# Kernel tuning notes

Hardware: AMD Instinct MI355X
Metric: run time of the kernel (lower is better)

Reference implementation:

```python
import jax, jax.numpy as jnp
import numpy as np

N_NODES = 50000
N_EDGES = 800000
FEAT = 64
HID = 128
N_TYPES = 4
N_REL = 3
N_LAYERS = 2
LN_EPS = 1e-5


def setup_inputs() -> dict:
    key = jax.random.key(0)
    ks = jax.random.split(key, 20)
    inp = {
        "z": jax.random.randint(ks[0], (N_NODES,), 0, 100, dtype=jnp.int32),
        "node_type": jax.random.randint(ks[1], (N_NODES,), 0, N_TYPES, dtype=jnp.int32),
        "edge_index": jax.random.randint(ks[2], (2, N_EDGES), 0, N_NODES, dtype=jnp.int32),
        "edge_type": jax.random.randint(ks[3], (N_EDGES,), 0, N_REL, dtype=jnp.int32),
        # learned parameters
        "z_embed": jax.random.normal(ks[4], (100, FEAT), jnp.float32),
        "enc_w1": jax.random.normal(ks[5], (N_TYPES, FEAT, HID), jnp.float32) * 0.05,
        "enc_b1": jnp.zeros((N_TYPES, HID), jnp.float32),
        "enc_w2": jax.random.normal(ks[6], (N_TYPES, HID, HID), jnp.float32) * 0.05,
        "enc_b2": jnp.zeros((N_TYPES, HID), jnp.float32),
        "lin_w": jax.random.normal(ks[7], (N_LAYERS, HID, HID), jnp.float32) * 0.05,
        "lin_b": jnp.zeros((N_LAYERS, HID), jnp.float32),
        "rel_w": jax.random.normal(ks[8], (N_LAYERS, N_REL, HID, HID), jnp.float32) * 0.05,
        "ln_g": jnp.ones((N_LAYERS, HID), jnp.float32),
        "ln_b": jnp.zeros((N_LAYERS, HID), jnp.float32),
        "reg_w": jax.random.normal(ks[9], (HID, 1), jnp.float32) * 0.05,
        "reg_b": jnp.zeros((1,), jnp.float32),
    }
    return inp


def _layer_norm(x, g, b):
    mu = jnp.mean(x, axis=-1, keepdims=True)
    var = jnp.mean((x - mu) ** 2, axis=-1, keepdims=True)
    return (x - mu) * jax.lax.rsqrt(var + LN_EPS) * g + b


def reference(z, node_type, edge_index, edge_type, z_embed, enc_w1, enc_b1,
              enc_w2, enc_b2, lin_w, lin_b, rel_w, ln_g, ln_b, reg_w, reg_b):
    n = z.shape[0]
    # FeatureBuilder (site_ads=None path): atomic-number embedding lookup
    raw = z_embed[z]  # [N, FEAT]
    # TypeSpecificEncoder: run all 4 type MLPs, select per node by node_type
    h = jax.nn.relu(jnp.einsum('nd,tdh->nth', raw, enc_w1) + enc_b1)  # [N,T,H]
    enc_all = jnp.einsum('nth,tho->nto', h, enc_w2) + enc_b2           # [N,T,H]
    x = jnp.take_along_axis(enc_all, node_type[:, None, None].astype(jnp.int32), axis=1)[:, 0, :]

    src, dst = edge_index[0], edge_index[1]
    deg = jax.ops.segment_sum(jnp.ones((edge_type.shape[0],), x.dtype), dst, num_segments=n)
    deg = jnp.clip(deg, 1.0, None)[:, None]  # [N,1]

    for l in range(N_LAYERS):
        out = jnp.zeros_like(x)
        x_src = x[src]  # [E, H] gathered source features
        for r in range(N_REL):
            mask = (edge_type == r).astype(x.dtype)[:, None]
            msg = (x_src * mask) @ rel_w[l, r]  # [E, H]
            out = out + jax.ops.segment_sum(msg, dst, num_segments=n)
        out = out / deg
        x = _layer_norm(x @ lin_w[l] + lin_b[l] + out, ln_g[l], ln_b[l])

    pooled = jnp.mean(x, axis=0)  # mean pooling, mask = all ones
    return pooled @ reg_w + reg_b  # [1]
```

## Files before the change

### kernel.cpp

```cpp
#include <hip/hip_runtime.h>

#define N_NODES 50000
#define N_EDGES 800000
#define FEAT 64
#define HID 128
#define N_TYPES 4
#define N_REL 3
#define N_LAYERS 2
#define LN_EPS 1e-5f
#define NROWS 50016
#define NG32 1563
#define CAP 64
#define NBKT 196
#define CAP1 4608
#define EPB 4096
#define BINCAP 56
#define NCOMBO 400
#define WT_STRIDE 136

typedef __attribute__((ext_vector_type(8))) short bf16x8;
typedef __attribute__((ext_vector_type(16))) float f32x16;
typedef __attribute__((ext_vector_type(2))) float f32x2;

static __device__ inline unsigned short f2bf(float f) {
    unsigned int u = __float_as_uint(f);
    return (unsigned short)((u + 0x7fffu + ((u >> 16) & 1u)) >> 16);
}
static __device__ inline unsigned int packbf2(float lo, float hi) {
    return (unsigned int)f2bf(lo) | ((unsigned int)f2bf(hi) << 16);
}

static __device__ inline void acc8_fp8w(float* a, unsigned int wx, unsigned int wy) {
    f32x2 d0 = __builtin_amdgcn_cvt_pk_f32_fp8((int)wx, false);
    f32x2 d1 = __builtin_amdgcn_cvt_pk_f32_fp8((int)wx, true);
    f32x2 d2 = __builtin_amdgcn_cvt_pk_f32_fp8((int)wy, false);
    f32x2 d3 = __builtin_amdgcn_cvt_pk_f32_fp8((int)wy, true);
    a[0] += d0[0]; a[1] += d0[1]; a[2] += d1[0]; a[3] += d1[1];
    a[4] += d2[0]; a[5] += d2[1]; a[6] += d3[0]; a[7] += d3[1];
}
static __device__ inline void acc16_fp8(float* a, uint4 w) {
    acc8_fp8w(a, w.x, w.y);
    acc8_fp8w(a + 8, w.z, w.w);
}

__global__ __launch_bounds__(256) void build_tables_kernel(
    const int* __restrict__ src, const int* __restrict__ dst,
    const int* __restrict__ et, const int* __restrict__ z,
    const int* __restrict__ nt,
    const float* __restrict__ z_embed, const float* __restrict__ w1,
    const float* __restrict__ b1, const float* __restrict__ w2,
    const float* __restrict__ b2, const float* __restrict__ rel_w,
    const float* __restrict__ lin_w, const float* __restrict__ lin_b,
    unsigned short* __restrict__ combo, int* __restrict__ bcnt,
    int* __restrict__ bucket, unsigned int* __restrict__ ytab,
    float* __restrict__ lintab, unsigned short* __restrict__ wbuf,
    float* __restrict__ pooled) {
    __shared__ int lbin[NBKT * BINCAP];
    __shared__ int lcnt[NBKT];
    __shared__ int lbase[NBKT];
    __shared__ float h[HID];
    __shared__ float xrow[HID];
    __shared__ float tmp[HID];

    int b = blockIdx.x;
    if (b < NBKT) {
        int ci = b * 256 + threadIdx.x;
        if (ci < N_NODES) combo[ci] = (unsigned short)(z[ci] * 4 + nt[ci]);
        for (int i = threadIdx.x; i < NBKT; i += 256) lcnt[i] = 0;
        __syncthreads();
        int base = b * EPB;
#pragma unroll
        for (int i = 0; i < EPB / 256; ++i) {
            int e = base + i * 256 + threadIdx.x;
            if (e < N_EDGES) {
                int d = dst[e];
                int bk = d >> 8;
                int v = src[e] | (et[e] << 16) | ((d & 255) << 18);
                int pos = atomicAdd(&lcnt[bk], 1);
                if (pos < BINCAP) lbin[bk * BINCAP + pos] = v;
            }
        }
        __syncthreads();
        if (threadIdx.x < NBKT) {
            int c = min(lcnt[threadIdx.x], BINCAP);
            lcnt[threadIdx.x] = c;
            lbase[threadIdx.x] = atomicAdd(&bcnt[threadIdx.x], c);
        }
        __syncthreads();
        int wv = threadIdx.x >> 6, ln = threadIdx.x & 63;
        for (int bb = wv; bb < NBKT; bb += 4) {
            int c = lcnt[bb];
            if (ln < c) {
                int gp = lbase[bb] + ln;
                if (gp < CAP1) bucket[bb * CAP1 + gp] = lbin[bb * BINCAP + ln];
            }
        }
        return;
    }
    if (b >= NBKT + NCOMBO) {
        int pb = b - (NBKT + NCOMBO);
        if (pb == 0 && threadIdx.x < HID) pooled[threadIdx.x] = 0.0f;
        int idx = pb * 256 + threadIdx.x;
        int k = idx & 127;
        int col = (idx >> 7) & 127;
        int mat = idx >> 14;
        float w = (mat < 3) ? rel_w[(((size_t)(3 + mat)) * HID + k) * HID + col]
                            : lin_w[((size_t)(HID + k)) * HID + col];
        wbuf[(size_t)mat * HID * WT_STRIDE + col * WT_STRIDE + k] = f2bf(w);
        return;
    }
    int c = b - NBKT;
    int zi = c >> 2;
    int t = c & 3;
    int j = threadIdx.x;
    bool act = j < HID;
    if (act) {
        float acc = b1[t * HID + j];
#pragma unroll 8
        for (int k = 0; k < FEAT; ++k)
            acc = fmaf(z_embed[zi * FEAT + k], w1[((size_t)t * FEAT + k) * HID + j], acc);
        h[j] = fmaxf(acc, 0.0f);
    }
    __syncthreads();
    if (act) {
        float acc2 = b2[t * HID + j];
#pragma unroll 8
        for (int k = 0; k < HID; ++k)
            acc2 = fmaf(h[k], w2[(size_t)t * HID * HID + k * HID + j], acc2);
        xrow[j] = acc2;
    }
    __syncthreads();
#pragma unroll 1
    for (int r = 0; r < N_REL; ++r) {
        if (act) {
            float a = 0.f;
            const float* W = rel_w + (size_t)r * HID * HID;
#pragma unroll 8
            for (int k = 0; k < HID; ++k) a = fmaf(xrow[k], W[k * HID + j], a);
            tmp[j] = a;
        }
        __syncthreads();
        if (j < 32) {
            int w0 = __builtin_amdgcn_cvt_pk_fp8_f32(tmp[4 * j], tmp[4 * j + 1], 0, false);
            w0 = __builtin_amdgcn_cvt_pk_fp8_f32(tmp[4 * j + 2], tmp[4 * j + 3], w0, true);
            ytab[(r * NCOMBO + c) * 32 + j] = (unsigned)w0;
        }
        __syncthreads();
    }
    if (act) {
        float a = lin_b[j];
#pragma unroll 8
        for (int k = 0; k < HID; ++k) a = fmaf(xrow[k], lin_w[k * HID + j], a);
        lintab[c * HID + j] = a;
    }
}

__global__ __launch_bounds__(256) void build2_kernel(const int* __restrict__ bcnt,
                                                     const int* __restrict__ bucket,
                                                     const unsigned short* __restrict__ combo,
                                                     int* __restrict__ cnt3,
                                                     int* __restrict__ payload) {
    __shared__ int lcnt[256 * 3];
    for (int i = threadIdx.x; i < 768; i += 256) lcnt[i] = 0;
    __syncthreads();
    int b = blockIdx.x;
    int n0 = b << 8;
    int cb = min(bcnt[b], CAP1);
    const int* bk = bucket + b * CAP1;
    for (int i = threadIdx.x; i < cb; i += 256) {
        int v = bk[i];
        atomicAdd(&lcnt[((v >> 18) & 255) * 3 + ((v >> 16) & 3)], 1);
    }
    __syncthreads();
    int t = threadIdx.x;
    int c0 = min(lcnt[t * 3 + 0], CAP);
    int c1 = min(lcnt[t * 3 + 1], CAP - c0);
    int c2 = min(lcnt[t * 3 + 2], CAP - c0 - c1);
    __syncthreads();
    lcnt[t * 3 + 0] = 0;
    lcnt[t * 3 + 1] = c0;
    lcnt[t * 3 + 2] = c0 + c1;
    int node = n0 + t;
    if (node < N_NODES) cnt3[node] = c0 | (c1 << 8) | (c2 << 16);
    __syncthreads();
    for (int i = threadIdx.x; i < cb; i += 256) {
        int v = bk[i];
        int dl = (v >> 18) & 255;
        int r = (v >> 16) & 3;
        int sc = v & 0xffff;
        int pos = atomicAdd(&lcnt[dl * 3 + r], 1);
        if (pos < CAP)
            payload[((n0 + dl) << 6) + pos] = sc | ((int)combo[sc] << 18);
    }
}

__global__ __launch_bounds__(256) void gather_ln1_kernel(
    const int* __restrict__ cnt3, const int* __restrict__ payload,
    const uint4* __restrict__ ytab16, const float* __restrict__ lintab,
    const unsigned short* __restrict__ combo, const float* __restrict__ lng,
    const float* __restrict__ lnb, uint4* __restrict__ xb4,
    uint4* __restrict__ xf8) {
    int tid = blockIdx.x * 256 + threadIdx.x;
    int node = tid >> 3;
    int l8 = tid & 7;
    bool real = node < N_NODES;
    int c3 = real ? cnt3[node] : 0;
    int c0 = c3 & 255, c1 = (c3 >> 8) & 255, c2 = (c3 >> 16) & 255;
    int tot = c0 + c1 + c2;
    float inv = 1.0f / (float)max(tot, 1);
    const int* pl = payload + (node << 6);
    float a[16] = {};
    int e = 0;
#pragma unroll 1
    for (int r = 0; r < 3; ++r) {
        int e1 = (r == 0) ? c0 : (r == 1) ? c0 + c1 : tot;
        int base = (r * NCOMBO) << 3;
        for (; e + 4 <= e1; e += 4) {
            int pA = pl[e], pB = pl[e + 1], pC = pl[e + 2], pD = pl[e + 3];
            uint4 vA = ytab16[base + ((pA >> 18) << 3) + l8];
            uint4 vB = ytab16[base + ((pB >> 18) << 3) + l8];
            uint4 vC = ytab16[base + ((pC >> 18) << 3) + l8];
            uint4 vD = ytab16[base + ((pD >> 18) << 3) + l8];
            acc16_fp8(a, vA);
            acc16_fp8(a, vB);
            acc16_fp8(a, vC);
            acc16_fp8(a, vD);
        }
        if (e + 2 <= e1) {
            int pA = pl[e], pB = pl[e + 1];
            uint4 vA = ytab16[base + ((pA >> 18) << 3) + l8];
            uint4 vB = ytab16[base + ((pB >> 18) << 3) + l8];
            acc16_fp8(a, vA);
            acc16_fp8(a, vB);
            e += 2;
        }
        if (e < e1) {
            int p = pl[e]; ++e;
            acc16_fp8(a, ytab16[base + ((p >> 18) << 3) + l8]);
        }
    }
    int cidx = real ? (int)combo[node] : 0;
    const float* lrow = lintab + cidx * HID + l8 * 16;
    float v[16], s = 0.f, q = 0.f;
#pragma unroll
    for (int j = 0; j < 16; ++j) {
        v[j] = fmaf(a[j], inv, lrow[j]);
        s += v[j];
        q += v[j] * v[j];
    }
#pragma unroll
    for (int mk = 1; mk < 8; mk <<= 1) {
        s += __shfl_xor(s, mk);
        q += __shfl_xor(q, mk);
    }
    float mu = s * (1.0f / HID);
    float rstd = rsqrtf(q * (1.0f / HID) - mu * mu + LN_EPS);
    const float* g16 = lng + l8 * 16;
    const float* b16 = lnb + l8 * 16;
    float o[16];
#pragma unroll
    for (int j = 0; j < 16; ++j) {
        o[j] = (v[j] - mu) * rstd * g16[j] + b16[j];
        if (!real) o[j] = 0.0f;
    }
    uint4 w0, w1;
    w0.x = packbf2(o[0], o[1]);   w0.y = packbf2(o[2], o[3]);
    w0.z = packbf2(o[4], o[5]);   w0.w = packbf2(o[6], o[7]);
    w1.x = packbf2(o[8], o[9]);   w1.y = packbf2(o[10], o[11]);
    w1.z = packbf2(o[12], o[13]); w1.w = packbf2(o[14], o[15]);
    xb4[(node << 4) + l8 * 2] = w0;
    xb4[(node << 4) + l8 * 2 + 1] = w1;
    int f0 = 0, f1 = 0, f2 = 0, f3 = 0;
    f0 = __builtin_amdgcn_cvt_pk_fp8_f32(o[0], o[1], f0, false);
    f0 = __builtin_amdgcn_cvt_pk_fp8_f32(o[2], o[3], f0, true);
    f1 = __builtin_amdgcn_cvt_pk_fp8_f32(o[4], o[5], f1, false);
    f1 = __builtin_amdgcn_cvt_pk_fp8_f32(o[6], o[7], f1, true);
    f2 = __builtin_amdgcn_cvt_pk_fp8_f32(o[8], o[9], f2, false);
    f2 = __builtin_amdgcn_cvt_pk_fp8_f32(o[10], o[11], f2, true);
    f3 = __builtin_amdgcn_cvt_pk_fp8_f32(o[12], o[13], f3, false);
    f3 = __builtin_amdgcn_cvt_pk_fp8_f32(o[14], o[15], f3, true);
    uint4 wf; wf.x = (unsigned)f0; wf.y = (unsigned)f1; wf.z = (unsigned)f2; wf.w = (unsigned)f3;
    xf8[(node << 3) + l8] = wf;
}

__global__ __launch_bounds__(256) void gather3_kernel(const int* __restrict__ cnt3,
                                                      const int* __restrict__ payload,
                                                      const uint4* __restrict__ xf8,
                                                      uint4* __restrict__ s0,
                                                      uint4* __restrict__ s1,
                                                      uint4* __restrict__ s2) {
    int tid = blockIdx.x * 256 + threadIdx.x;
    int node = tid >> 3;
    int l8 = tid & 7;
    bool real = node < N_NODES;
    int c3 = real ? cnt3[node] : 0;
    int c0 = c3 & 255, c1 = (c3 >> 8) & 255, c2 = (c3 >> 16) & 255;
    int tot = c0 + c1 + c2;
    float inv = 1.0f / (float)max(tot, 1);
    const int* pl = payload + (node << 6);
    int o = (node << 4) + l8 * 2;
    int e = 0;
#pragma unroll 1
    for (int r = 0; r < 3; ++r) {
        int e1 = (r == 0) ? c0 : (r == 1) ? c0 + c1 : tot;
        float a[16] = {};
        for (; e + 4 <= e1; e += 4) {
            int pA = pl[e], pB = pl[e + 1], pC = pl[e + 2], pD = pl[e + 3];
            uint4 vA = xf8[((pA & 0xffff) << 3) + l8];
            uint4 vB = xf8[((pB & 0xffff) << 3) + l8];
            uint4 vC = xf8[((pC & 0xffff) << 3) + l8];
            uint4 vD = xf8[((pD & 0xffff) << 3) + l8];
            acc16_fp8(a, vA);
            acc16_fp8(a, vB);
            acc16_fp8(a, vC);
            acc16_fp8(a, vD);
        }
        if (e + 2 <= e1) {
            int pA = pl[e], pB = pl[e + 1];
            uint4 vA = xf8[((pA & 0xffff) << 3) + l8];
            uint4 vB = xf8[((pB & 0xffff) << 3) + l8];
            acc16_fp8(a, vA);
            acc16_fp8(a, vB);
            e += 2;
        }
        if (e < e1) {
            int p = pl[e]; ++e;
            acc16_fp8(a, xf8[((p & 0xffff) << 3) + l8]);
        }
        uint4 w0, w1;
        w0.x = packbf2(a[0] * inv, a[1] * inv);
        w0.y = packbf2(a[2] * inv, a[3] * inv);
        w0.z = packbf2(a[4] * inv, a[5] * inv);
        w0.w = packbf2(a[6] * inv, a[7] * inv);
        w1.x = packbf2(a[8] * inv, a[9] * inv);
        w1.y = packbf2(a[10] * inv, a[11] * inv);
        w1.z = packbf2(a[12] * inv, a[13] * inv);
        w1.w = packbf2(a[14] * inv, a[15] * inv);
        if (r == 0) { s0[o] = w0; s0[o + 1] = w1; }
        else if (r == 1) { s1[o] = w0; s1[o + 1] = w1; }
        else { s2[o] = w0; s2[o + 1] = w1; }
    }
}

__global__ __launch_bounds__(512) void fused_layer_kernel(
    const unsigned short* __restrict__ s0, const unsigned short* __restrict__ s1,
    const unsigned short* __restrict__ s2, const unsigned short* __restrict__ xb,
    const uint4* __restrict__ wbuf, const float* __restrict__ lb,
    const float* __restrict__ lng, const float* __restrict__ lnb,
    float* __restrict__ pooled, const float* __restrict__ reg_w,
    const float* __restrict__ reg_b, float* __restrict__ out,
    int* __restrict__ done) {
    __shared__ __align__(16) unsigned short Wt[4 * HID * WT_STRIDE];
    __shared__ float csh[3 * HID];
    __shared__ float pooled_sh[HID];
    __shared__ int lastFlag;

    int wave = threadIdx.x >> 6;
    int lane = threadIdx.x & 63;
    int n32 = lane & 31;
    int hf = lane >> 5;

    int g0 = wave * gridDim.x + blockIdx.x;
    bool active = g0 < NG32;
    size_t rofs = active ? ((size_t)(g0 * 32 + n32) * HID + hf * 8) : 0;

    bf16x8 bufA[8], bufB[8];
    {
        const unsigned short* p0 = s0 + rofs;
#pragma unroll
        for (int t = 0; t < 8; ++t) bufA[t] = *(const bf16x8*)(p0 + t * 16);
    }

    if (threadIdx.x < HID) {
        pooled_sh[threadIdx.x] = 0.0f;
        csh[threadIdx.x] = lb[threadIdx.x];
        csh[HID + threadIdx.x] = lng[threadIdx.x];
        csh[2 * HID + threadIdx.x] = lnb[threadIdx.x];
    }
    uint4* wt4 = (uint4*)Wt;
#pragma unroll
    for (int i = 0; i < 17; ++i)
        wt4[i * 512 + threadIdx.x] = wbuf[i * 512 + threadIdx.x];
    __syncthreads();

    float pacc[4] = {0.f, 0.f, 0.f, 0.f};

    if (active) {
        f32x16 acc[4];
#pragma unroll
        for (int ct = 0; ct < 4; ++ct)
#pragma unroll
            for (int i = 0; i < 16; ++i) acc[ct][i] = 0.0f;

        const unsigned short* wbase = Wt + n32 * WT_STRIDE + hf * 8;

#define DOMAT(buf, m)                                                          \
        {                                                                      \
            const unsigned short* wm = wbase + (m) * (HID * WT_STRIDE);        \
            _Pragma("unroll")                                                  \
            for (int t = 0; t < 8; ++t) {                                      \
                _Pragma("unroll")                                              \
                for (int ct = 0; ct < 4; ++ct) {                               \
                    bf16x8 bfr = *(const bf16x8*)(wm + ct * 32 * WT_STRIDE + t * 16); \
                    acc[ct] = __builtin_amdgcn_mfma_f32_32x32x16_bf16(         \
                        buf[t], bfr, acc[ct], 0, 0, 0);                        \
                }                                                              \
            }                                                                  \
        }
#define LDMAT(buf, srcp)                                                       \
        {                                                                      \
            const unsigned short* _p = (srcp) + rofs;                          \
            _Pragma("unroll")                                                  \
            for (int t = 0; t < 8; ++t) buf[t] = *(const bf16x8*)(_p + t * 16);\
        }

        LDMAT(bufB, s1);
        DOMAT(bufA, 0);
        LDMAT(bufA, s2);
        DOMAT(bufB, 1);
        LDMAT(bufB, xb);
        DOMAT(bufA, 2);
        DOMAT(bufB, 3);
#undef DOMAT
#undef LDMAT

        int node0 = g0 * 32;
#pragma unroll
        for (int reg = 0; reg < 16; ++reg) {
            int row = node0 + (reg & 3) + 8 * (reg >> 2) + 4 * hf;
            float v[4];
            float s = 0.f, q = 0.f;
#pragma unroll
            for (int ct = 0; ct < 4; ++ct) {
                v[ct] = acc[ct][reg] + csh[ct * 32 + n32];
                s += v[ct];
                q += v[ct] * v[ct];
            }
#pragma unroll
            for (int mk = 1; mk < 32; mk <<= 1) {
                s += __shfl_xor(s, mk);
                q += __shfl_xor(q, mk);
            }
            float mu = s * (1.0f / HID);
            float rstd = rsqrtf(q * (1.0f / HID) - mu * mu + LN_EPS);
            if (row < N_NODES) {
#pragma unroll
                for (int ct = 0; ct < 4; ++ct) {
                    int col = ct * 32 + n32;
                    pacc[ct] += (v[ct] - mu) * rstd * csh[HID + col] + csh[2 * HID + col];
                }
            }
        }
    }

#pragma unroll
    for (int ct = 0; ct < 4; ++ct) {
        float t = pacc[ct] + __shfl_xor(pacc[ct], 32);
        if (hf == 0) atomicAdd(&pooled_sh[ct * 32 + n32], t);
    }
    __syncthreads();
    if (threadIdx.x < HID) atomicAdd(&pooled[threadIdx.x], pooled_sh[threadIdx.x]);

    __threadfence();
    __syncthreads();
    if (threadIdx.x == 0)
        lastFlag = (atomicAdd(done, 1) == (int)gridDim.x - 1);
    __syncthreads();
    if (lastFlag && threadIdx.x < 64) {
        int l = threadIdx.x;
        float s = atomicAdd(&pooled[l], 0.0f) * reg_w[l] +
                  atomicAdd(&pooled[64 + l], 0.0f) * reg_w[64 + l];
#pragma unroll
        for (int o = 32; o; o >>= 1) s += __shfl_down(s, o);
        if (l == 0) out[0] = s * (1.0f / N_NODES) + reg_b[0];
    }
}

extern "C" void kernel_launch(void* const* d_in, const int* in_sizes, int n_in,
                              void* d_out, int out_size, void* d_ws, size_t ws_size,
                              hipStream_t stream) {
    const int* z = (const int*)d_in[0];
    const int* nt = (const int*)d_in[1];
    const int* ei = (const int*)d_in[2];
    const int* et = (const int*)d_in[3];
    const float* z_embed = (const float*)d_in[4];
    const float* enc_w1 = (const float*)d_in[5];
    const float* enc_b1 = (const float*)d_in[6];
    const float* enc_w2 = (const float*)d_in[7];
    const float* enc_b2 = (const float*)d_in[8];
    const float* lin_w = (const float*)d_in[9];
    const float* lin_b = (const float*)d_in[10];
    const float* rel_w = (const float*)d_in[11];
    const float* ln_g = (const float*)d_in[12];
    const float* ln_b = (const float*)d_in[13];
    const float* reg_w = (const float*)d_in[14];
    const float* reg_b = (const float*)d_in[15];
    float* out = (float*)d_out;

    const size_t NHb = (size_t)NROWS * HID;
    char* p = (char*)d_ws;
    unsigned short* xb = (unsigned short*)p;    p += NHb * 2;
    unsigned short* s0 = (unsigned short*)p;    p += NHb * 2;
    unsigned short* s1 = (unsigned short*)p;    p += NHb * 2;
    unsigned short* s2 = (unsigned short*)p;    p += NHb * 2;
    uint4* xf8 = (uint4*)p;                     p += NHb;
    unsigned short* wbuf = (unsigned short*)p;  p += (size_t)4 * HID * WT_STRIDE * 2;
    unsigned int* ytab = (unsigned int*)p;      p += (size_t)N_REL * NCOMBO * HID;
    float* lintab = (float*)p;                  p += NCOMBO * HID * 4;
    unsigned short* combo = (unsigned short*)p; p += N_NODES * 2;
    float* pooled = (float*)p;                  p += HID * 4;
    int* cnt3 = (int*)p;                        p += N_NODES * 4;
    int* bcnt = (int*)p;                        p += NBKT * 4;
    int* done = (int*)p;                        p += 4;
    int* bucket = (int*)p;                      p += (size_t)NBKT * CAP1 * 4;
    int* payload = (int*)p;                     p += (size_t)N_NODES * CAP * 4;

    const int* src = ei;
    const int* dst = ei + N_EDGES;

    hipMemsetAsync(bcnt, 0, (NBKT + 1) * sizeof(int), stream);

    build_tables_kernel<<<NBKT + NCOMBO + 256, 256, 0, stream>>>(
        src, dst, et, z, nt, z_embed, enc_w1, enc_b1, enc_w2, enc_b2,
        rel_w, lin_w, lin_b, combo, bcnt, bucket, ytab, lintab, wbuf, pooled);

    build2_kernel<<<NBKT, 256, 0, stream>>>(bcnt, bucket, combo, cnt3, payload);

    gather_ln1_kernel<<<1563, 256, 0, stream>>>(cnt3, payload, (const uint4*)ytab, lintab,
                                                combo, ln_g, ln_b, (uint4*)xb, xf8);
    gather3_kernel<<<1563, 256, 0, stream>>>(cnt3, payload, xf8,
                                             (uint4*)s0, (uint4*)s1, (uint4*)s2);
    fused_layer_kernel<<<256, 512, 0, stream>>>(
        s0, s1, s2, xb, (const uint4*)wbuf, lin_b + HID, ln_g + HID, ln_b + HID,
        pooled, reg_w, reg_b, out, done);
}
```

Baseline: 238.2 us.

## Apply layer-2 relation weights before the edge gather instead of after

Layer 2 now multiplies node features by the three relation matrices and the linear weight first, in a new MFMA kernel. A second kernel then gathers the transformed bf16 rows per edge and fuses the degree normalisation, bias, LayerNorm and pooling. This removes the fp8 feature copy, the three per-relation aggregate buffers and the 512-thread fused GEMM kernel. In exchange each edge gathers bf16 rows that are twice the size of the old fp8 rows, and a float linear-part buffer is written and re-read. Pooling now goes through per-element shared-memory atomics into eight global partial copies to spread contention.

```diff
diff --git a/kernel.cpp b/kernel.cpp
--- a/kernel.cpp
+++ b/kernel.cpp
@@ -41,6 +41,16 @@
 static __device__ inline void acc16_fp8(float* a, uint4 w) {
     acc8_fp8w(a, w.x, w.y);
     acc8_fp8w(a + 8, w.z, w.w);
+}
+static __device__ inline void accbf16x8(float* a, uint4 w) {
+    a[0] += __uint_as_float(w.x << 16);
+    a[1] += __uint_as_float(w.x & 0xffff0000u);
+    a[2] += __uint_as_float(w.y << 16);
+    a[3] += __uint_as_float(w.y & 0xffff0000u);
+    a[4] += __uint_as_float(w.z << 16);
+    a[5] += __uint_as_float(w.z & 0xffff0000u);
+    a[6] += __uint_as_float(w.w << 16);
+    a[7] += __uint_as_float(w.w & 0xffff0000u);
 }
 
 __global__ __launch_bounds__(256) void build_tables_kernel(
@@ -99,7 +109,7 @@
     }
     if (b >= NBKT + NCOMBO) {
         int pb = b - (NBKT + NCOMBO);
-        if (pb == 0 && threadIdx.x < HID) pooled[threadIdx.x] = 0.0f;
+        if (pb < 4) pooled[pb * 256 + threadIdx.x] = 0.0f;
         int idx = pb * 256 + threadIdx.x;
         int k = idx & 127;
         int col = (idx >> 7) & 127;
@@ -198,8 +208,7 @@
     const int* __restrict__ cnt3, const int* __restrict__ payload,
     const uint4* __restrict__ ytab16, const float* __restrict__ lintab,
     const unsigned short* __restrict__ combo, const float* __restrict__ lng,
-    const float* __restrict__ lnb, uint4* __restrict__ xb4,
-    uint4* __restrict__ xf8) {
+    const float* __restrict__ lnb, uint4* __restrict__ xb4) {
     int tid = blockIdx.x * 256 + threadIdx.x;
     int node = tid >> 3;
     int l8 = tid & 7;
@@ -270,25 +279,88 @@
     w1.z = packbf2(o[12], o[13]); w1.w = packbf2(o[14], o[15]);
     xb4[(node << 4) + l8 * 2] = w0;
     xb4[(node << 4) + l8 * 2 + 1] = w1;
-    int f0 = 0, f1 = 0, f2 = 0, f3 = 0;
-    f0 = __builtin_amdgcn_cvt_pk_fp8_f32(o[0], o[1], f0, false);
-    f0 = __builtin_amdgcn_cvt_pk_fp8_f32(o[2], o[3], f0, true);
-    f1 = __builtin_amdgcn_cvt_pk_fp8_f32(o[4], o[5], f1, false);
-    f1 = __builtin_amdgcn_cvt_pk_fp8_f32(o[6], o[7], f1, true);
-    f2 = __builtin_amdgcn_cvt_pk_fp8_f32(o[8], o[9], f2, false);
-    f2 = __builtin_amdgcn_cvt_pk_fp8_f32(o[10], o[11], f2, true);
-    f3 = __builtin_amdgcn_cvt_pk_fp8_f32(o[12], o[13], f3, false);
-    f3 = __builtin_amdgcn_cvt_pk_fp8_f32(o[14], o[15], f3, true);
-    uint4 wf; wf.x = (unsigned)f0; wf.y = (unsigned)f1; wf.z = (unsigned)f2; wf.w = (unsigned)f3;
-    xf8[(node << 3) + l8] = wf;
-}
-
-__global__ __launch_bounds__(256) void gather3_kernel(const int* __restrict__ cnt3,
-                                                      const int* __restrict__ payload,
-                                                      const uint4* __restrict__ xf8,
-                                                      uint4* __restrict__ s0,
-                                                      uint4* __restrict__ s1,
-                                                      uint4* __restrict__ s2) {
+}
+
+__global__ __launch_bounds__(256) void ygemm_kernel(
+    const unsigned short* __restrict__ xb, const uint4* __restrict__ wbuf,
+    unsigned int* __restrict__ y0, unsigned int* __restrict__ y1,
+    unsigned int* __restrict__ y2, float* __restrict__ linpart) {
+    __shared__ __align__(16) unsigned short Wm[HID * WT_STRIDE];
+    int wave = threadIdx.x >> 6, lane = threadIdx.x & 63;
+    int n32 = lane & 31, hf = lane >> 5;
+    int mat = blockIdx.x / 391;
+    int g = (blockIdx.x - mat * 391) * 4 + wave;
+    bool active = g < NG32;
+    int node = g * 32 + n32;
+    size_t rofs = active ? ((size_t)node * HID + hf * 8) : 0;
+    bf16x8 bfrag[8];
+    {
+        const unsigned short* p = xb + rofs;
+#pragma unroll
+        for (int t = 0; t < 8; ++t) bfrag[t] = *(const bf16x8*)(p + t * 16);
+    }
+    const uint4* wsrc = wbuf + (size_t)mat * (HID * WT_STRIDE / 8);
+    uint4* wd = (uint4*)Wm;
+#pragma unroll
+    for (int i = 0; i < 9; ++i) {
+        int idx = i * 256 + threadIdx.x;
+        if (idx < HID * WT_STRIDE / 8) wd[idx] = wsrc[idx];
+    }
+    __syncthreads();
+    if (!active) return;
+    f32x16 acc[4];
+#pragma unroll
+    for (int ct = 0; ct < 4; ++ct)
+#pragma unroll
+        for (int i = 0; i < 16; ++i) acc[ct][i] = 0.0f;
+    const unsigned short* wbase = Wm + n32 * WT_STRIDE + hf * 8;
+#pragma unroll
+    for (int t = 0; t < 8; ++t)
+#pragma unroll
+        for (int ct = 0; ct < 4; ++ct) {
+            bf16x8 afr = *(const bf16x8*)(wbase + ct * 32 * WT_STRIDE + t * 16);
+            acc[ct] = __builtin_amdgcn_mfma_f32_32x32x16_bf16(afr, bfrag[t], acc[ct], 0, 0, 0);
+        }
+    if (mat < 3) {
+        unsigned int* yr = (mat == 0) ? y0 : (mat == 1) ? y1 : y2;
+        unsigned int* yp = yr + (size_t)node * 64;
+#pragma unroll
+        for (int ct = 0; ct < 4; ++ct)
+#pragma unroll
+            for (int q = 0; q < 4; ++q) {
+                int f0 = ct * 32 + 8 * q + 4 * hf;
+                uint2 w;
+                w.x = packbf2(acc[ct][4 * q + 0], acc[ct][4 * q + 1]);
+                w.y = packbf2(acc[ct][4 * q + 2], acc[ct][4 * q + 3]);
+                *(uint2*)(yp + (f0 >> 1)) = w;
+            }
+    } else {
+        float* lp = linpart + (size_t)node * HID;
+#pragma unroll
+        for (int ct = 0; ct < 4; ++ct)
+#pragma unroll
+            for (int q = 0; q < 4; ++q) {
+                int f0 = ct * 32 + 8 * q + 4 * hf;
+                float4 w;
+                w.x = acc[ct][4 * q + 0]; w.y = acc[ct][4 * q + 1];
+                w.z = acc[ct][4 * q + 2]; w.w = acc[ct][4 * q + 3];
+                *(float4*)(lp + f0) = w;
+            }
+    }
+}
+
+__global__ __launch_bounds__(256) void gather_ln2_kernel(
+    const int* __restrict__ cnt3, const int* __restrict__ payload,
+    const uint4* __restrict__ y0, const uint4* __restrict__ y1,
+    const uint4* __restrict__ y2, const float* __restrict__ linpart,
+    const float* __restrict__ lb, const float* __restrict__ lng,
+    const float* __restrict__ lnb, float* __restrict__ pooled,
+    const float* __restrict__ reg_w, const float* __restrict__ reg_b,
+    float* __restrict__ out, int* __restrict__ done) {
+    __shared__ float pooled_sh[HID];
+    __shared__ int lastFlag;
+    if (threadIdx.x < HID) pooled_sh[threadIdx.x] = 0.0f;
+    __syncthreads();
     int tid = blockIdx.x * 256 + threadIdx.x;
     int node = tid >> 3;
     int l8 = tid & 7;
@@ -298,168 +370,62 @@
     int tot = c0 + c1 + c2;
     float inv = 1.0f / (float)max(tot, 1);
     const int* pl = payload + (node << 6);
-    int o = (node << 4) + l8 * 2;
+    const float* lpp = linpart + (size_t)node * HID + l8 * 16;
+    float4 lp0 = *(const float4*)(lpp);
+    float4 lp1 = *(const float4*)(lpp + 4);
+    float4 lp2 = *(const float4*)(lpp + 8);
+    float4 lp3 = *(const float4*)(lpp + 12);
+    float a[16] = {};
     int e = 0;
 #pragma unroll 1
     for (int r = 0; r < 3; ++r) {
         int e1 = (r == 0) ? c0 : (r == 1) ? c0 + c1 : tot;
-        float a[16] = {};
-        for (; e + 4 <= e1; e += 4) {
-            int pA = pl[e], pB = pl[e + 1], pC = pl[e + 2], pD = pl[e + 3];
-            uint4 vA = xf8[((pA & 0xffff) << 3) + l8];
-            uint4 vB = xf8[((pB & 0xffff) << 3) + l8];
-            uint4 vC = xf8[((pC & 0xffff) << 3) + l8];
-            uint4 vD = xf8[((pD & 0xffff) << 3) + l8];
-            acc16_fp8(a, vA);
-            acc16_fp8(a, vB);
-            acc16_fp8(a, vC);
-            acc16_fp8(a, vD);
-        }
-        if (e + 2 <= e1) {
-            int pA = pl[e], pB = pl[e + 1];
-            uint4 vA = xf8[((pA & 0xffff) << 3) + l8];
-            uint4 vB = xf8[((pB & 0xffff) << 3) + l8];
-            acc16_fp8(a, vA);
-            acc16_fp8(a, vB);
-            e += 2;
+        const uint4* yt = (r == 0) ? y0 : (r == 1) ? y1 : y2;
+        for (; e + 2 <= e1; e += 2) {
+            int pA = pl[e] & 0xffff, pB = pl[e + 1] & 0xffff;
+            uint4 vA0 = yt[pA * 16 + l8 * 2];
+            uint4 vA1 = yt[pA * 16 + l8 * 2 + 1];
+            uint4 vB0 = yt[pB * 16 + l8 * 2];
+            uint4 vB1 = yt[pB * 16 + l8 * 2 + 1];
+            accbf16x8(a, vA0); accbf16x8(a + 8, vA1);
+            accbf16x8(a, vB0); accbf16x8(a + 8, vB1);
         }
         if (e < e1) {
-            int p = pl[e]; ++e;
-            acc16_fp8(a, xf8[((p & 0xffff) << 3) + l8]);
-        }
-        uint4 w0, w1;
-        w0.x = packbf2(a[0] * inv, a[1] * inv);
-        w0.y = packbf2(a[2] * inv, a[3] * inv);
-        w0.z = packbf2(a[4] * inv, a[5] * inv);
-        w0.w = packbf2(a[6] * inv, a[7] * inv);
-        w1.x = packbf2(a[8] * inv, a[9] * inv);
-        w1.y = packbf2(a[10] * inv, a[11] * inv);
-        w1.z = packbf2(a[12] * inv, a[13] * inv);
-        w1.w = packbf2(a[14] * inv, a[15] * inv);
-        if (r == 0) { s0[o] = w0; s0[o + 1] = w1; }
-        else if (r == 1) { s1[o] = w0; s1[o + 1] = w1; }
-        else { s2[o] = w0; s2[o + 1] = w1; }
-    }
-}
-
-__global__ __launch_bounds__(512) void fused_layer_kernel(
-    const unsigned short* __restrict__ s0, const unsigned short* __restrict__ s1,
-    const unsigned short* __restrict__ s2, const unsigned short* __restrict__ xb,
-    const uint4* __restrict__ wbuf, const float* __restrict__ lb,
-    const float* __restrict__ lng, const float* __restrict__ lnb,
-    float* __restrict__ pooled, const float* __restrict__ reg_w,
-    const float* __restrict__ reg_b, float* __restrict__ out,
-    int* __restrict__ done) {
-    __shared__ __align__(16) unsigned short Wt[4 * HID * WT_STRIDE];
-    __shared__ float csh[3 * HID];
-    __shared__ float pooled_sh[HID];
-    __shared__ int lastFlag;
-
-    int wave = threadIdx.x >> 6;
-    int lane = threadIdx.x & 63;
-    int n32 = lane & 31;
-    int hf = lane >> 5;
-
-    int g0 = wave * gridDim.x + blockIdx.x;
-    bool active = g0 < NG32;
-    size_t rofs = active ? ((size_t)(g0 * 32 + n32) * HID + hf * 8) : 0;
-
-    bf16x8 bufA[8], bufB[8];
-    {
-        const unsigned short* p0 = s0 + rofs;
-#pragma unroll
-        for (int t = 0; t < 8; ++t) bufA[t] = *(const bf16x8*)(p0 + t * 16);
-    }
-
-    if (threadIdx.x < HID) {
-        pooled_sh[threadIdx.x] = 0.0f;
-        csh[threadIdx.x] = lb[threadIdx.x];
-        csh[HID + threadIdx.x] = lng[threadIdx.x];
-        csh[2 * HID + threadIdx.x] = lnb[threadIdx.x];
-    }
-    uint4* wt4 = (uint4*)Wt;
-#pragma unroll
-    for (int i = 0; i < 17; ++i)
-        wt4[i * 512 + threadIdx.x] = wbuf[i * 512 + threadIdx.x];
-    __syncthreads();
-
-    float pacc[4] = {0.f, 0.f, 0.f, 0.f};
-
-    if (active) {
-        f32x16 acc[4];
-#pragma unroll
-        for (int ct = 0; ct < 4; ++ct)
-#pragma unroll
-            for (int i = 0; i < 16; ++i) acc[ct][i] = 0.0f;
-
-        const unsigned short* wbase = Wt + n32 * WT_STRIDE + hf * 8;
-
-#define DOMAT(buf, m)                                                          \
-        {                                                                      \
-            const unsigned short* wm = wbase + (m) * (HID * WT_STRIDE);        \
-            _Pragma("unroll")                                                  \
-            for (int t = 0; t < 8; ++t) {                                      \
-                _Pragma("unroll")                                              \
-                for (int ct = 0; ct < 4; ++ct) {                               \
-                    bf16x8 bfr = *(const bf16x8*)(wm + ct * 32 * WT_STRIDE + t * 16); \
-                    acc[ct] = __builtin_amdgcn_mfma_f32_32x32x16_bf16(         \
-                        buf[t], bfr, acc[ct], 0, 0, 0);                        \
-                }                                                              \
-            }                                                                  \
-        }
-#define LDMAT(buf, srcp)                                                       \
-        {                                                                      \
-            const unsigned short* _p = (srcp) + rofs;                          \
-            _Pragma("unroll")                                                  \
-            for (int t = 0; t < 8; ++t) buf[t] = *(const bf16x8*)(_p + t * 16);\
-        }
-
-        LDMAT(bufB, s1);
-        DOMAT(bufA, 0);
-        LDMAT(bufA, s2);
-        DOMAT(bufB, 1);
-        LDMAT(bufB, xb);
-        DOMAT(bufA, 2);
-        DOMAT(bufB, 3);
-#undef DOMAT
-#undef LDMAT
-
-        int node0 = g0 * 32;
-#pragma unroll
-        for (int reg = 0; reg < 16; ++reg) {
-            int row = node0 + (reg & 3) + 8 * (reg >> 2) + 4 * hf;
-            float v[4];
-            float s = 0.f, q = 0.f;
-#pragma unroll
-            for (int ct = 0; ct < 4; ++ct) {
-                v[ct] = acc[ct][reg] + csh[ct * 32 + n32];
-                s += v[ct];
-                q += v[ct] * v[ct];
-            }
-#pragma unroll
-            for (int mk = 1; mk < 32; mk <<= 1) {
-                s += __shfl_xor(s, mk);
-                q += __shfl_xor(q, mk);
-            }
-            float mu = s * (1.0f / HID);
-            float rstd = rsqrtf(q * (1.0f / HID) - mu * mu + LN_EPS);
-            if (row < N_NODES) {
-#pragma unroll
-                for (int ct = 0; ct < 4; ++ct) {
-                    int col = ct * 32 + n32;
-                    pacc[ct] += (v[ct] - mu) * rstd * csh[HID + col] + csh[2 * HID + col];
-                }
-            }
-        }
-    }
-
-#pragma unroll
-    for (int ct = 0; ct < 4; ++ct) {
-        float t = pacc[ct] + __shfl_xor(pacc[ct], 32);
-        if (hf == 0) atomicAdd(&pooled_sh[ct * 32 + n32], t);
-    }
-    __syncthreads();
-    if (threadIdx.x < HID) atomicAdd(&pooled[threadIdx.x], pooled_sh[threadIdx.x]);
+            int p = pl[e] & 0xffff; ++e;
+            uint4 v0 = yt[p * 16 + l8 * 2];
+            uint4 v1 = yt[p * 16 + l8 * 2 + 1];
+            accbf16x8(a, v0); accbf16x8(a + 8, v1);
+        }
+    }
+    float lpv[16] = {lp0.x, lp0.y, lp0.z, lp0.w, lp1.x, lp1.y, lp1.z, lp1.w,
+                     lp2.x, lp2.y, lp2.z, lp2.w, lp3.x, lp3.y, lp3.z, lp3.w};
+    const float* lbp = lb + l8 * 16;
+    float v[16], s = 0.f, q = 0.f;
+#pragma unroll
+    for (int j = 0; j < 16; ++j) {
+        v[j] = fmaf(a[j], inv, lpv[j] + lbp[j]);
+        s += v[j];
+        q += v[j] * v[j];
+    }
+#pragma unroll
+    for (int mk = 1; mk < 8; mk <<= 1) {
+        s += __shfl_xor(s, mk);
+        q += __shfl_xor(q, mk);
+    }
+    float mu = s * (1.0f / HID);
+    float rstd = rsqrtf(q * (1.0f / HID) - mu * mu + LN_EPS);
+    const float* g16 = lng + l8 * 16;
+    const float* b16 = lnb + l8 * 16;
+    if (real) {
+#pragma unroll
+        for (int j = 0; j < 16; ++j) {
+            float o = (v[j] - mu) * rstd * g16[j] + b16[j];
+            atomicAdd(&pooled_sh[l8 * 16 + j], o);
+        }
+    }
+    __syncthreads();
+    if (threadIdx.x < HID)
+        atomicAdd(&pooled[(blockIdx.x & 7) * HID + threadIdx.x], pooled_sh[threadIdx.x]);
 
     __threadfence();
     __syncthreads();
@@ -468,11 +434,14 @@
     __syncthreads();
     if (lastFlag && threadIdx.x < 64) {
         int l = threadIdx.x;
-        float s = atomicAdd(&pooled[l], 0.0f) * reg_w[l] +
-                  atomicAdd(&pooled[64 + l], 0.0f) * reg_w[64 + l];
-#pragma unroll
-        for (int o = 32; o; o >>= 1) s += __shfl_down(s, o);
-        if (l == 0) out[0] = s * (1.0f / N_NODES) + reg_b[0];
+        float s2 = 0.f;
+#pragma unroll
+        for (int k = 0; k < 8; ++k)
+            s2 += atomicAdd(&pooled[k * HID + l], 0.0f) * reg_w[l] +
+                  atomicAdd(&pooled[k * HID + 64 + l], 0.0f) * reg_w[64 + l];
+#pragma unroll
+        for (int o2 = 32; o2; o2 >>= 1) s2 += __shfl_down(s2, o2);
+        if (l == 0) out[0] = s2 * (1.0f / N_NODES) + reg_b[0];
     }
 }
 
@@ -500,15 +469,15 @@
     const size_t NHb = (size_t)NROWS * HID;
     char* p = (char*)d_ws;
     unsigned short* xb = (unsigned short*)p;    p += NHb * 2;
-    unsigned short* s0 = (unsigned short*)p;    p += NHb * 2;
-    unsigned short* s1 = (unsigned short*)p;    p += NHb * 2;
-    unsigned short* s2 = (unsigned short*)p;    p += NHb * 2;
-    uint4* xf8 = (uint4*)p;                     p += NHb;
+    unsigned short* y0 = (unsigned short*)p;    p += NHb * 2;
+    unsigned short* y1 = (unsigned short*)p;    p += NHb * 2;
+    unsigned short* y2 = (unsigned short*)p;    p += NHb * 2;
+    float* linpart = (float*)p;                 p += NHb * 4;
     unsigned short* wbuf = (unsigned short*)p;  p += (size_t)4 * HID * WT_STRIDE * 2;
     unsigned int* ytab = (unsigned int*)p;      p += (size_t)N_REL * NCOMBO * HID;
     float* lintab = (float*)p;                  p += NCOMBO * HID * 4;
     unsigned short* combo = (unsigned short*)p; p += N_NODES * 2;
-    float* pooled = (float*)p;                  p += HID * 4;
+    float* pooled = (float*)p;                  p += 8 * HID * 4;
     int* cnt3 = (int*)p;                        p += N_NODES * 4;
     int* bcnt = (int*)p;                        p += NBKT * 4;
     int* done = (int*)p;                        p += 4;
@@ -527,10 +496,12 @@
     build2_kernel<<<NBKT, 256, 0, stream>>>(bcnt, bucket, combo, cnt3, payload);
 
     gather_ln1_kernel<<<1563, 256, 0, stream>>>(cnt3, payload, (const uint4*)ytab, lintab,
-                                                combo, ln_g, ln_b, (uint4*)xb, xf8);
-    gather3_kernel<<<1563, 256, 0, stream>>>(cnt3, payload, xf8,
-                                             (uint4*)s0, (uint4*)s1, (uint4*)s2);
-    fused_layer_kernel<<<256, 512, 0, stream>>>(
-        s0, s1, s2, xb, (const uint4*)wbuf, lin_b + HID, ln_g + HID, ln_b + HID,
-        pooled, reg_w, reg_b, out, done);
-}
+                                                combo, ln_g, ln_b, (uint4*)xb);
+    ygemm_kernel<<<4 * 391, 256, 0, stream>>>(xb, (const uint4*)wbuf,
+                                              (unsigned int*)y0, (unsigned int*)y1,
+                                              (unsigned int*)y2, linpart);
+    gather_ln2_kernel<<<1563, 256, 0, stream>>>(
+        cnt3, payload, (const uint4*)y0, (const uint4*)y1, (const uint4*)y2,
+        linpart, lin_b + HID, ln_g + HID, ln_b + HID, pooled,
+        reg_w, reg_b, out, done);
+}
```

Result: slower. 335.3 us (+40.8%).
